# Performance work log

Measured on AMD Instinct MI355X. Metric: run time of the kernel, lower is better.

## Reference

```python
import jax, jax.numpy as jnp
import numpy as np


def setup_inputs() -> dict:
    key = jax.random.key(0)
    k1, k2 = jax.random.split(key)
    return {
        "embeddings": jax.random.normal(k1, (4, 768, 32, 32), dtype=jnp.float32),
        "database": jax.random.normal(k2, (20000, 768), dtype=jnp.float32),
        "k": 3,
        "out_h": 512,
        "out_w": 512,
    }


def reference(embeddings, database, k, out_h, out_w):
    # embeddings: [B, D, h, w]  (segmenter hidden state), database: [N, D]
    B, D, h, w = embeddings.shape
    # B x h x w x D -> B x (h*w) x D query layout, as in _get_ood_scores
    q = jnp.transpose(embeddings, (0, 2, 3, 1)).reshape(B, h * w, D)
    # squared Euclidean distances via (||q||^2 + ||x||^2 - 2 q.x)
    q2 = jnp.sum(q * q, axis=-1)[..., None]                 # [B, hw, 1]
    x2 = jnp.sum(database * database, axis=-1)[None, None]  # [1, 1, N]
    d2 = q2 + x2 - 2.0 * jnp.einsum("bqd,nd->bqn", q, database)
    dist = jnp.sqrt(jnp.maximum(d2, 1e-12))                 # [B, hw, N]
    # k smallest distances (sklearn kneighbors) then mean over neighbors
    neg_topk, _ = jax.lax.top_k(-dist, k)                   # [B, hw, k]
    ood = jnp.mean(-neg_topk, axis=-1).reshape(B, h, w)
    # F.interpolate(..., mode='bilinear', align_corners=False) == half-pixel bilinear
    ood_up = jax.image.resize(ood[:, None], (B, 1, out_h, out_w), method="bilinear")
    return ood_up
```

## Files before the change

kernel.cpp:

```cpp
#include <hip/hip_runtime.h>
#include <hip/hip_bf16.h>
#include <math.h>

constexpr int B    = 4;
constexpr int D    = 768;
constexpr int HW   = 1024;
constexpr int M    = B * HW;
constexpr int NDB  = 20000;
constexpr int LT   = 158;
constexpr int NDBP = LT * 128;
constexpr int OUTH = 512;
constexpr int OUTW = 512;

constexpr int BM     = 256;
constexpr int BN     = 128;
constexpr int KSTEPS = D / 64;
constexpr int GSTEPS = KSTEPS / 2;
constexpr int NSPLIT = 16;
constexpr int NT2    = 79;
constexpr int STEPB  = 128 * 64;

typedef int   i32x8  __attribute__((ext_vector_type(8)));
typedef float f32x16 __attribute__((ext_vector_type(16)));

__device__ __forceinline__ void insert3(float& t0, float& t1, float& t2, float d) {
    float a0 = fminf(d, t0);
    float b0 = fmaxf(d, t0);
    float a1 = fminf(b0, t1);
    float b1 = fmaxf(b0, t1);
    t0 = a0; t1 = a1;
    t2 = fminf(b1, t2);
}

__device__ __forceinline__ unsigned int pack4_fp8(float a, float b, float c, float d) {
    int v = __builtin_amdgcn_cvt_pk_fp8_f32(a, b, 0, false);
    v = __builtin_amdgcn_cvt_pk_fp8_f32(c, d, v, true);
    return (unsigned int)v;
}

__device__ __forceinline__ void gl_lds16(const unsigned char* g, unsigned char* l) {
    __builtin_amdgcn_global_load_lds(
        (const __attribute__((address_space(1))) void*)g,
        (__attribute__((address_space(3))) void*)l, 16, 0, 0);
}

__global__ __launch_bounds__(256) void db_convert(const float* __restrict__ db,
                                                  uint4* __restrict__ dbt8,
                                                  float* __restrict__ x2p) {
    __shared__ float panel[128][65];
    __shared__ float part[512];
    const int lt = blockIdx.x;
    const int g  = blockIdx.y;
    const int t  = threadIdx.x;
    const int n0 = lt * 128;

    #pragma unroll
    for (int pass = 0; pass < 8; ++pass) {
        int idx = pass * 256 + t;
        int row = idx >> 4, c4 = idx & 15;
        int n = n0 + row;
        float4 v = make_float4(0.f, 0.f, 0.f, 0.f);
        if (n < NDB) v = *(const float4*)(db + (size_t)n * D + g * 64 + c4 * 4);
        panel[row][c4 * 4 + 0] = v.x;
        panel[row][c4 * 4 + 1] = v.y;
        panel[row][c4 * 4 + 2] = v.z;
        panel[row][c4 * 4 + 3] = v.w;
    }
    __syncthreads();
    #pragma unroll
    for (int pass = 0; pass < 2; ++pass) {
        int idx = pass * 256 + t;
        int r  = idx & 31;
        int kc = (idx >> 5) & 1;
        int h2 = (idx >> 6) & 1;
        int rg = idx >> 7;
        int row  = rg * 32 + r;
        int kloc = kc * 32 + h2 * 16;
        float v[16];
        float ss = 0.f;
        #pragma unroll
        for (int j = 0; j < 16; ++j) {
            v[j] = panel[row][kloc + j];
            ss = fmaf(v[j], v[j], ss);
        }
        uint4 o;
        o.x = pack4_fp8(v[0],  v[1],  v[2],  v[3]);
        o.y = pack4_fp8(v[4],  v[5],  v[6],  v[7]);
        o.z = pack4_fp8(v[8],  v[9],  v[10], v[11]);
        o.w = pack4_fp8(v[12], v[13], v[14], v[15]);
        dbt8[((size_t)lt * KSTEPS + g) * 512 + idx] = o;
        part[idx] = ss;
    }
    __syncthreads();
    if (t < 128) {
        int base = (t >> 5) * 128 + (t & 31);
        float s = part[base] + part[base + 32] + part[base + 64] + part[base + 96];
        x2p[((size_t)lt * KSTEPS + g) * 128 + t] = s;
    }
}

__global__ __launch_bounds__(256) void x2_reduce(const float* __restrict__ x2p,
                                                 float* __restrict__ x2) {
    int n = blockIdx.x * 256 + threadIdx.x;
    if (n >= NDBP) return;
    if (n >= NDB) { x2[n] = 1e30f; return; }
    const float* p = x2p + (size_t)(n >> 7) * KSTEPS * 128 + (n & 127);
    float s = 0.f;
    #pragma unroll
    for (int g = 0; g < KSTEPS; ++g) s += p[g * 128];
    x2[n] = s;
}

__global__ __launch_bounds__(256) void q_convert(const float* __restrict__ emb,
                                                 uint4* __restrict__ qbt8,
                                                 float* __restrict__ q2p) {
    __shared__ float part[512];
    const int qt = blockIdx.x;
    const int g  = blockIdx.y;
    const int t  = threadIdx.x;
    const int b  = qt >> 3;
    const int p0 = (qt & 7) * 128;

    #pragma unroll
    for (int pass = 0; pass < 2; ++pass) {
        int idx = pass * 256 + t;
        int r  = idx & 31;
        int kc = (idx >> 5) & 1;
        int h2 = (idx >> 6) & 1;
        int rg = idx >> 7;
        int prow = rg * 32 + r;
        int kb = g * 64 + kc * 32 + h2 * 16;
        const float* src = emb + ((size_t)b * D + kb) * HW + p0 + prow;
        float v[16];
        float ss = 0.f;
        #pragma unroll
        for (int j = 0; j < 16; ++j) {
            v[j] = src[(size_t)j * HW];
            ss = fmaf(v[j], v[j], ss);
        }
        uint4 o;
        o.x = pack4_fp8(-2.f*v[0],  -2.f*v[1],  -2.f*v[2],  -2.f*v[3]);
        o.y = pack4_fp8(-2.f*v[4],  -2.f*v[5],  -2.f*v[6],  -2.f*v[7]);
        o.z = pack4_fp8(-2.f*v[8],  -2.f*v[9],  -2.f*v[10], -2.f*v[11]);
        o.w = pack4_fp8(-2.f*v[12], -2.f*v[13], -2.f*v[14], -2.f*v[15]);
        qbt8[((size_t)qt * KSTEPS + g) * 512 + idx] = o;
        part[idx] = ss;
    }
    __syncthreads();
    if (t < 128) {
        int base = (t >> 5) * 128 + (t & 31);
        float s = part[base] + part[base + 32] + part[base + 64] + part[base + 96];
        q2p[((size_t)qt * KSTEPS + g) * 128 + t] = s;
    }
}

__global__ __launch_bounds__(256, 2) void gemm_topk(const unsigned char* __restrict__ dbt8,
                                                    const unsigned char* __restrict__ qbt8,
                                                    const float* __restrict__ x2g,
                                                    float* __restrict__ partials) {
    __shared__ __align__(16) unsigned char As[4 * STEPB];
    __shared__ __align__(16) unsigned char Bs[2 * STEPB];
    __shared__ float X2s[BM];
    __shared__ float red[4][BN][3];

    const int tid  = threadIdx.x;
    const int lane = tid & 63;
    const int w    = tid >> 6;
    const int lts  = w >> 1;
    const int wr   = w & 1;
    const int h    = lane >> 5;
    const int l31  = lane & 31;

    const int bid   = blockIdx.x;
    const int xcd   = bid & 7;
    const int j     = bid >> 3;
    const int sp    = xcd + 8 * (j >> 5);
    const int qtile = j & 31;
    const int m0    = qtile * BN;

    int a_off[2], b_off[4];
    #pragma unroll
    for (int i = 0; i < 2; ++i) a_off[i] = lts * 16384 + (wr * 2 + i) * 2048 + h * 512 + l31 * 16;
    #pragma unroll
    for (int j4 = 0; j4 < 4; ++j4) b_off[j4] = j4 * 2048 + h * 512 + l31 * 16;

    const int lb = lane * 16;
    const unsigned char* qstep0 = qbt8 + ((size_t)qtile * KSTEPS + lts) * STEPB + wr * 4096 + lb;
    unsigned char* bdst = Bs + lts * 8192 + wr * 4096;
    unsigned char* adst = As + w * 8192;

    float t0[4], t1[4], t2[4];
    #pragma unroll
    for (int j4 = 0; j4 < 4; ++j4) { t0[j4] = INFINITY; t1[j4] = INFINITY; t2[j4] = INFINITY; }

    for (int tile = sp; tile < NT2; tile += NSPLIT) {
        const int n0 = tile * BM;
        const unsigned char* astep = dbt8 + (((size_t)(2 * tile + lts) * KSTEPS) + wr) * STEPB + lb;
        const unsigned char* bstep = qstep0;

        f32x16 acc[2][4];
        #pragma unroll
        for (int i = 0; i < 2; ++i)
            #pragma unroll
            for (int j4 = 0; j4 < 4; ++j4)
                #pragma unroll
                for (int r = 0; r < 16; ++r) acc[i][j4][r] = 0.f;

        for (int g2 = 0; g2 < GSTEPS; ++g2) {
            __syncthreads();
            #pragma unroll
            for (int l = 0; l < 8; ++l) gl_lds16(astep + l * 1024, adst + l * 1024);
            #pragma unroll
            for (int l = 0; l < 4; ++l) gl_lds16(bstep + l * 1024, bdst + l * 1024);
            if (g2 == 0) X2s[tid] = x2g[n0 + tid];
            astep += 2 * STEPB;
            bstep += 2 * STEPB;
            __syncthreads();

            #pragma unroll
            for (int s = 0; s < 2; ++s) {
                i32x8 af[2], bf[4];
                #pragma unroll
                for (int i = 0; i < 2; ++i) {
                    int4 lo = *(const int4*)(As + s * 8192 + a_off[i]);
                    int4 hi = *(const int4*)(As + s * 8192 + a_off[i] + 1024);
                    af[i] = (i32x8){lo.x, lo.y, lo.z, lo.w, hi.x, hi.y, hi.z, hi.w};
                }
                #pragma unroll
                for (int j4 = 0; j4 < 4; ++j4) {
                    int4 lo = *(const int4*)(Bs + s * 8192 + b_off[j4]);
                    int4 hi = *(const int4*)(Bs + s * 8192 + b_off[j4] + 1024);
                    bf[j4] = (i32x8){lo.x, lo.y, lo.z, lo.w, hi.x, hi.y, hi.z, hi.w};
                }
                #pragma unroll
                for (int i = 0; i < 2; ++i)
                    #pragma unroll
                    for (int j4 = 0; j4 < 4; ++j4)
                        acc[i][j4] = __builtin_amdgcn_mfma_scale_f32_32x32x64_f8f6f4(
                            af[i], bf[j4], acc[i][j4], 0, 0,
                            0, 0x7f7f7f7f, 0, 0x7f7f7f7f);
            }
        }

        #pragma unroll
        for (int i = 0; i < 2; ++i) {
            #pragma unroll
            for (int rg2 = 0; rg2 < 4; ++rg2) {
                float4 xv = *(const float4*)&X2s[w * 64 + i * 32 + rg2 * 8 + 4 * h];
                #pragma unroll
                for (int j4 = 0; j4 < 4; ++j4) {
                    #pragma unroll
                    for (int rr = 0; rr < 4; ++rr) {
                        float s = acc[i][j4][rg2 * 4 + rr] + ((const float*)&xv)[rr];
                        insert3(t0[j4], t1[j4], t2[j4], s);
                    }
                }
            }
        }
    }

    #pragma unroll
    for (int j4 = 0; j4 < 4; ++j4) {
        float o0 = __shfl_xor(t0[j4], 32);
        float o1 = __shfl_xor(t1[j4], 32);
        float o2 = __shfl_xor(t2[j4], 32);
        insert3(t0[j4], t1[j4], t2[j4], o0);
        insert3(t0[j4], t1[j4], t2[j4], o1);
        insert3(t0[j4], t1[j4], t2[j4], o2);
    }
    if (h == 0) {
        #pragma unroll
        for (int j4 = 0; j4 < 4; ++j4) {
            int col = j4 * 32 + l31;
            red[w][col][0] = t0[j4];
            red[w][col][1] = t1[j4];
            red[w][col][2] = t2[j4];
        }
    }
    __syncthreads();
    if (tid < BN) {
        float a0 = red[0][tid][0], a1 = red[0][tid][1], a2 = red[0][tid][2];
        #pragma unroll
        for (int ww = 1; ww < 4; ++ww) {
            insert3(a0, a1, a2, red[ww][tid][0]);
            insert3(a0, a1, a2, red[ww][tid][1]);
            insert3(a0, a1, a2, red[ww][tid][2]);
        }
        float* dst = partials + ((size_t)(m0 + tid) * NSPLIT + sp) * 3;
        dst[0] = a0; dst[1] = a1; dst[2] = a2;
    }
}

__global__ __launch_bounds__(256) void merge_ood(const float* __restrict__ partials,
                                                 const float* __restrict__ q2p,
                                                 float* __restrict__ ood) {
    int m = blockIdx.x * 256 + threadIdx.x;
    if (m >= M) return;
    const float* pp = partials + (size_t)m * NSPLIT * 3;
    float a0 = INFINITY, a1 = INFINITY, a2 = INFINITY;
    #pragma unroll
    for (int j = 0; j < NSPLIT * 3; ++j) insert3(a0, a1, a2, pp[j]);
    const float* qp = q2p + (size_t)(m >> 7) * KSTEPS * 128 + (m & 127);
    float q = 0.f;
    #pragma unroll
    for (int g = 0; g < KSTEPS; ++g) q += qp[g * 128];
    float d0 = sqrtf(fmaxf(q + a0, 1e-12f));
    float d1 = sqrtf(fmaxf(q + a1, 1e-12f));
    float d2 = sqrtf(fmaxf(q + a2, 1e-12f));
    ood[m] = (d0 + d1 + d2) * (1.f / 3.f);
}

__global__ __launch_bounds__(256) void upsample(const float* __restrict__ ood,
                                                float* __restrict__ out) {
    int idx = blockIdx.x * 256 + threadIdx.x;
    int ox = idx & (OUTW - 1);
    int oy = (idx >> 9) & (OUTH - 1);
    int bb = idx >> 18;
    float sx = (ox + 0.5f) * (32.f / OUTW) - 0.5f;
    float sy = (oy + 0.5f) * (32.f / OUTH) - 0.5f;
    float fx = floorf(sx), fy = floorf(sy);
    float wx = sx - fx, wy = sy - fy;
    int x0 = max(0, min(31, (int)fx));
    int x1 = max(0, min(31, (int)fx + 1));
    int y0 = max(0, min(31, (int)fy));
    int y1 = max(0, min(31, (int)fy + 1));
    const float* src = ood + bb * 1024;
    float v00 = src[y0 * 32 + x0];
    float v01 = src[y0 * 32 + x1];
    float v10 = src[y1 * 32 + x0];
    float v11 = src[y1 * 32 + x1];
    float top = v00 + wx * (v01 - v00);
    float bot = v10 + wx * (v11 - v10);
    out[idx] = top + wy * (bot - top);
}

extern "C" void kernel_launch(void* const* d_in, const int* in_sizes, int n_in,
                              void* d_out, int out_size, void* d_ws, size_t ws_size,
                              hipStream_t stream) {
    const float* emb = (const float*)d_in[0];
    const float* db  = (const float*)d_in[1];
    float* out = (float*)d_out;

    char* ws = (char*)d_ws;
    unsigned char* dbt8 = (unsigned char*)ws;
    unsigned char* qbt8 = (unsigned char*)(ws + 15532032);
    float* x2       = (float*)(ws + 18677760);
    float* x2p      = (float*)(ws + 18758656);
    float* q2p      = (float*)(ws + 19729408);
    float* ood      = (float*)(ws + 19926016);
    float* partials = (float*)(ws + 19942400);

    db_convert<<<dim3(LT, KSTEPS), 256, 0, stream>>>(db, (uint4*)dbt8, x2p);
    q_convert<<<dim3(32, KSTEPS), 256, 0, stream>>>(emb, (uint4*)qbt8, q2p);
    x2_reduce<<<(NDBP + 255) / 256, 256, 0, stream>>>(x2p, x2);
    gemm_topk<<<NSPLIT * 32, 256, 0, stream>>>(dbt8, qbt8, x2, partials);
    merge_ood<<<(M + 255) / 256, 256, 0, stream>>>(partials, q2p, ood);
    upsample<<<(B * OUTH * OUTW) / 256, 256, 0, stream>>>(ood, out);
}
```

Baseline: 184.4 us.

## Double-buffer GEMM K-steps with prefetch, fold x2 reduction into GEMM, vectorize db_convert

Replaces the load-then-compute loop in gemm_topk with a double-buffered pipeline: each K-step issues async global-to-LDS loads for the next step (including across tile boundaries) while running MFMAs on the current buffer, using one barrier per step instead of two. The separate x2_reduce kernel is removed, and each tile now sums its per-group x2 partials inline, which saves a launch but repeats that reduction for every query tile. db_convert now uses float4 LDS stores and loads with a padded row of 68 floats. The aim is to hide global memory latency and reduce launch overhead, at the cost of smaller per-step LDS chunks and redundant x2 work.

```diff
diff --git a/kernel.cpp b/kernel.cpp
--- a/kernel.cpp
+++ b/kernel.cpp
@@ -15,7 +15,6 @@
 constexpr int BM     = 256;
 constexpr int BN     = 128;
 constexpr int KSTEPS = D / 64;
-constexpr int GSTEPS = KSTEPS / 2;
 constexpr int NSPLIT = 16;
 constexpr int NT2    = 79;
 constexpr int STEPB  = 128 * 64;
@@ -47,7 +46,7 @@
 __global__ __launch_bounds__(256) void db_convert(const float* __restrict__ db,
                                                   uint4* __restrict__ dbt8,
                                                   float* __restrict__ x2p) {
-    __shared__ float panel[128][65];
+    __shared__ float panel[128][68];
     __shared__ float part[512];
     const int lt = blockIdx.x;
     const int g  = blockIdx.y;
@@ -61,10 +60,7 @@
         int n = n0 + row;
         float4 v = make_float4(0.f, 0.f, 0.f, 0.f);
         if (n < NDB) v = *(const float4*)(db + (size_t)n * D + g * 64 + c4 * 4);
-        panel[row][c4 * 4 + 0] = v.x;
-        panel[row][c4 * 4 + 1] = v.y;
-        panel[row][c4 * 4 + 2] = v.z;
-        panel[row][c4 * 4 + 3] = v.w;
+        *(float4*)&panel[row][c4 * 4] = v;
     }
     __syncthreads();
     #pragma unroll
@@ -76,18 +72,19 @@
         int rg = idx >> 7;
         int row  = rg * 32 + r;
         int kloc = kc * 32 + h2 * 16;
-        float v[16];
-        float ss = 0.f;
-        #pragma unroll
-        for (int j = 0; j < 16; ++j) {
-            v[j] = panel[row][kloc + j];
-            ss = fmaf(v[j], v[j], ss);
-        }
+        float4 va = *(const float4*)&panel[row][kloc + 0];
+        float4 vb = *(const float4*)&panel[row][kloc + 4];
+        float4 vc = *(const float4*)&panel[row][kloc + 8];
+        float4 vd = *(const float4*)&panel[row][kloc + 12];
+        float ss = va.x*va.x + va.y*va.y + va.z*va.z + va.w*va.w
+                 + vb.x*vb.x + vb.y*vb.y + vb.z*vb.z + vb.w*vb.w
+                 + vc.x*vc.x + vc.y*vc.y + vc.z*vc.z + vc.w*vc.w
+                 + vd.x*vd.x + vd.y*vd.y + vd.z*vd.z + vd.w*vd.w;
         uint4 o;
-        o.x = pack4_fp8(v[0],  v[1],  v[2],  v[3]);
-        o.y = pack4_fp8(v[4],  v[5],  v[6],  v[7]);
-        o.z = pack4_fp8(v[8],  v[9],  v[10], v[11]);
-        o.w = pack4_fp8(v[12], v[13], v[14], v[15]);
+        o.x = pack4_fp8(va.x, va.y, va.z, va.w);
+        o.y = pack4_fp8(vb.x, vb.y, vb.z, vb.w);
+        o.z = pack4_fp8(vc.x, vc.y, vc.z, vc.w);
+        o.w = pack4_fp8(vd.x, vd.y, vd.z, vd.w);
         dbt8[((size_t)lt * KSTEPS + g) * 512 + idx] = o;
         part[idx] = ss;
     }
@@ -97,18 +94,6 @@
         float s = part[base] + part[base + 32] + part[base + 64] + part[base + 96];
         x2p[((size_t)lt * KSTEPS + g) * 128 + t] = s;
     }
-}
-
-__global__ __launch_bounds__(256) void x2_reduce(const float* __restrict__ x2p,
-                                                 float* __restrict__ x2) {
-    int n = blockIdx.x * 256 + threadIdx.x;
-    if (n >= NDBP) return;
-    if (n >= NDB) { x2[n] = 1e30f; return; }
-    const float* p = x2p + (size_t)(n >> 7) * KSTEPS * 128 + (n & 127);
-    float s = 0.f;
-    #pragma unroll
-    for (int g = 0; g < KSTEPS; ++g) s += p[g * 128];
-    x2[n] = s;
 }
 
 __global__ __launch_bounds__(256) void q_convert(const float* __restrict__ emb,
@@ -156,10 +141,10 @@
 
 __global__ __launch_bounds__(256, 2) void gemm_topk(const unsigned char* __restrict__ dbt8,
                                                     const unsigned char* __restrict__ qbt8,
-                                                    const float* __restrict__ x2g,
+                                                    const float* __restrict__ x2p,
                                                     float* __restrict__ partials) {
-    __shared__ __align__(16) unsigned char As[4 * STEPB];
-    __shared__ __align__(16) unsigned char Bs[2 * STEPB];
+    __shared__ __align__(16) unsigned char Asm[2 * 16384];
+    __shared__ __align__(16) unsigned char Bsm[2 * 8192];
     __shared__ float X2s[BM];
     __shared__ float red[4][BN][3];
 
@@ -180,23 +165,37 @@
 
     int a_off[2], b_off[4];
     #pragma unroll
-    for (int i = 0; i < 2; ++i) a_off[i] = lts * 16384 + (wr * 2 + i) * 2048 + h * 512 + l31 * 16;
+    for (int i = 0; i < 2; ++i) a_off[i] = lts * 8192 + (wr * 2 + i) * 2048 + h * 512 + l31 * 16;
     #pragma unroll
     for (int j4 = 0; j4 < 4; ++j4) b_off[j4] = j4 * 2048 + h * 512 + l31 * 16;
 
-    const int lb = lane * 16;
-    const unsigned char* qstep0 = qbt8 + ((size_t)qtile * KSTEPS + lts) * STEPB + wr * 4096 + lb;
-    unsigned char* bdst = Bs + lts * 8192 + wr * 4096;
-    unsigned char* adst = As + w * 8192;
+    const unsigned char* aNext = dbt8 + (size_t)(2 * sp + lts) * KSTEPS * STEPB + wr * 4096 + lane * 16;
+    const unsigned char* bNext = qbt8 + (size_t)qtile * KSTEPS * STEPB + w * 2048 + lane * 16;
+    unsigned char* aDst = Asm + w * 4096;
+    unsigned char* bDst = Bsm + w * 2048;
+
+    #pragma unroll
+    for (int l = 0; l < 4; ++l) gl_lds16(aNext + l * 1024, aDst + l * 1024);
+    #pragma unroll
+    for (int l = 0; l < 2; ++l) gl_lds16(bNext + l * 1024, bDst + l * 1024);
 
     float t0[4], t1[4], t2[4];
     #pragma unroll
     for (int j4 = 0; j4 < 4; ++j4) { t0[j4] = INFINITY; t1[j4] = INFINITY; t2[j4] = INFINITY; }
 
     for (int tile = sp; tile < NT2; tile += NSPLIT) {
-        const int n0 = tile * BM;
-        const unsigned char* astep = dbt8 + (((size_t)(2 * tile + lts) * KSTEPS) + wr) * STEPB + lb;
-        const unsigned char* bstep = qstep0;
+        __syncthreads();
+        {
+            int n = tile * BM + tid;
+            float s = 1e30f;
+            if (n < NDB) {
+                const float* p = x2p + (size_t)(n >> 7) * (KSTEPS * 128) + (n & 127);
+                s = 0.f;
+                #pragma unroll
+                for (int g = 0; g < KSTEPS; ++g) s += p[g * 128];
+            }
+            X2s[tid] = s;
+        }
 
         f32x16 acc[2][4];
         #pragma unroll
@@ -206,40 +205,53 @@
                 #pragma unroll
                 for (int r = 0; r < 16; ++r) acc[i][j4][r] = 0.f;
 
-        for (int g2 = 0; g2 < GSTEPS; ++g2) {
+        const bool lastTile = (tile + NSPLIT >= NT2);
+
+        #pragma unroll 2
+        for (int g = 0; g < KSTEPS; ++g) {
+            const int cur = g & 1;
             __syncthreads();
-            #pragma unroll
-            for (int l = 0; l < 8; ++l) gl_lds16(astep + l * 1024, adst + l * 1024);
-            #pragma unroll
-            for (int l = 0; l < 4; ++l) gl_lds16(bstep + l * 1024, bdst + l * 1024);
-            if (g2 == 0) X2s[tid] = x2g[n0 + tid];
-            astep += 2 * STEPB;
-            bstep += 2 * STEPB;
-            __syncthreads();
-
-            #pragma unroll
-            for (int s = 0; s < 2; ++s) {
-                i32x8 af[2], bf[4];
-                #pragma unroll
-                for (int i = 0; i < 2; ++i) {
-                    int4 lo = *(const int4*)(As + s * 8192 + a_off[i]);
-                    int4 hi = *(const int4*)(As + s * 8192 + a_off[i] + 1024);
-                    af[i] = (i32x8){lo.x, lo.y, lo.z, lo.w, hi.x, hi.y, hi.z, hi.w};
-                }
-                #pragma unroll
-                for (int j4 = 0; j4 < 4; ++j4) {
-                    int4 lo = *(const int4*)(Bs + s * 8192 + b_off[j4]);
-                    int4 hi = *(const int4*)(Bs + s * 8192 + b_off[j4] + 1024);
-                    bf[j4] = (i32x8){lo.x, lo.y, lo.z, lo.w, hi.x, hi.y, hi.z, hi.w};
-                }
-                #pragma unroll
-                for (int i = 0; i < 2; ++i)
-                    #pragma unroll
-                    for (int j4 = 0; j4 < 4; ++j4)
-                        acc[i][j4] = __builtin_amdgcn_mfma_scale_f32_32x32x64_f8f6f4(
-                            af[i], bf[j4], acc[i][j4], 0, 0,
-                            0, 0x7f7f7f7f, 0, 0x7f7f7f7f);
-            }
+            if (g < KSTEPS - 1) {
+                aNext += STEPB;
+                bNext += STEPB;
+                unsigned char* ad = aDst + (cur ^ 1) * 16384;
+                unsigned char* bd = bDst + (cur ^ 1) * 8192;
+                #pragma unroll
+                for (int l = 0; l < 4; ++l) gl_lds16(aNext + l * 1024, ad + l * 1024);
+                #pragma unroll
+                for (int l = 0; l < 2; ++l) gl_lds16(bNext + l * 1024, bd + l * 1024);
+            } else if (!lastTile) {
+                aNext += (size_t)(2 * NSPLIT) * KSTEPS * STEPB - (KSTEPS - 1) * STEPB;
+                bNext -= (size_t)(KSTEPS - 1) * STEPB;
+                unsigned char* ad = aDst + (cur ^ 1) * 16384;
+                unsigned char* bd = bDst + (cur ^ 1) * 8192;
+                #pragma unroll
+                for (int l = 0; l < 4; ++l) gl_lds16(aNext + l * 1024, ad + l * 1024);
+                #pragma unroll
+                for (int l = 0; l < 2; ++l) gl_lds16(bNext + l * 1024, bd + l * 1024);
+            }
+            const unsigned char* Ab = Asm + cur * 16384;
+            const unsigned char* Bb = Bsm + cur * 8192;
+            i32x8 af[2], bf[4];
+            #pragma unroll
+            for (int i = 0; i < 2; ++i) {
+                int4 lo = *(const int4*)(Ab + a_off[i]);
+                int4 hi = *(const int4*)(Ab + a_off[i] + 1024);
+                af[i] = (i32x8){lo.x, lo.y, lo.z, lo.w, hi.x, hi.y, hi.z, hi.w};
+            }
+            #pragma unroll
+            for (int j4 = 0; j4 < 4; ++j4) {
+                int4 lo = *(const int4*)(Bb + b_off[j4]);
+                int4 hi = *(const int4*)(Bb + b_off[j4] + 1024);
+                bf[j4] = (i32x8){lo.x, lo.y, lo.z, lo.w, hi.x, hi.y, hi.z, hi.w};
+            }
+            #pragma unroll
+            for (int i = 0; i < 2; ++i)
+                #pragma unroll
+                for (int j4 = 0; j4 < 4; ++j4)
+                    acc[i][j4] = __builtin_amdgcn_mfma_scale_f32_32x32x64_f8f6f4(
+                        af[i], bf[j4], acc[i][j4], 0, 0,
+                        0, 0x7f7f7f7f, 0, 0x7f7f7f7f);
         }
 
         #pragma unroll
@@ -344,16 +356,14 @@
     char* ws = (char*)d_ws;
     unsigned char* dbt8 = (unsigned char*)ws;
     unsigned char* qbt8 = (unsigned char*)(ws + 15532032);
-    float* x2       = (float*)(ws + 18677760);
-    float* x2p      = (float*)(ws + 18758656);
-    float* q2p      = (float*)(ws + 19729408);
-    float* ood      = (float*)(ws + 19926016);
-    float* partials = (float*)(ws + 19942400);
+    float* x2p      = (float*)(ws + 18677760);
+    float* q2p      = (float*)(ws + 19648512);
+    float* ood      = (float*)(ws + 19845120);
+    float* partials = (float*)(ws + 19861504);
 
     db_convert<<<dim3(LT, KSTEPS), 256, 0, stream>>>(db, (uint4*)dbt8, x2p);
     q_convert<<<dim3(32, KSTEPS), 256, 0, stream>>>(emb, (uint4*)qbt8, q2p);
-    x2_reduce<<<(NDBP + 255) / 256, 256, 0, stream>>>(x2p, x2);
-    gemm_topk<<<NSPLIT * 32, 256, 0, stream>>>(dbt8, qbt8, x2, partials);
+    gemm_topk<<<NSPLIT * 32, 256, 0, stream>>>(dbt8, qbt8, x2p, partials);
     merge_ood<<<(M + 255) / 256, 256, 0, stream>>>(partials, q2p, ood);
     upsample<<<(B * OUTH * OUTW) / 256, 256, 0, stream>>>(ood, out);
 }
```

Result: no change. 184.4 us (-0.0%).
